# Kernel tuning notes

Measured on AMD Instinct MI355X. Metric: run time of the kernel, lower is better.

Reference implementation:

```python
import jax, jax.numpy as jnp
import numpy as np

N, E, D, K, H = 100000, 1600000, 32, 3, 1


def setup_inputs() -> dict:
    key = jax.random.key(0)
    ks = jax.random.split(key, 7)
    return {
        "src": jax.random.randint(ks[0], (E,), 0, N),
        "dst": jax.random.randint(ks[1], (E,), 0, N),
        "embedding": jax.random.normal(ks[2], (N, D), jnp.float32),
        "lambda_max": jnp.full((1,), 2.0, jnp.float32),
        # ChebConv: single Linear(k*d -> d) over concatenated Chebyshev terms (shared by both calls)
        "cheb_W": jax.random.normal(ks[3], (K * D, D), jnp.float32) / np.sqrt(K * D),
        "cheb_b": jnp.zeros((D,), jnp.float32),
        # GATv2: fc_src / fc_dst Linear(d -> H*d) + attention vector (H, d)
        "gat_W_src": jax.random.normal(ks[4], (D, H * D), jnp.float32) / np.sqrt(D),
        "gat_b_src": jnp.zeros((H * D,), jnp.float32),
        "gat_W_dst": jax.random.normal(ks[5], (D, H * D), jnp.float32) / np.sqrt(D),
        "gat_b_dst": jnp.zeros((H * D,), jnp.float32),
        "gat_attn": jax.random.normal(ks[6], (H, D), jnp.float32) / np.sqrt(D),
    }


def _cheb(src, dst, feat, lam, W, b, n):
    # DGL ChebConv with lambda_max given; activation = leaky_relu (slope 0.01)
    deg = jnp.clip(jax.ops.segment_sum(jnp.ones(src.shape[0], feat.dtype), dst, num_segments=n), 1.0)
    dinv = deg[:, None] ** -0.5  # D^{-1/2}, (N,1)
    re_norm = 2.0 / lam[0]

    def unnL(f):  # D^{-1/2} A D^{-1/2} f
        return jax.ops.segment_sum((f * dinv)[src], dst, num_segments=n) * dinv

    X0 = feat
    X1 = -re_norm * unnL(X0) + X0 * (re_norm - 1.0)
    Xs = [X0, X1]
    for _ in range(2, K):
        Xi = -2.0 * re_norm * unnL(X1) + X1 * (2.0 * (re_norm - 1.0)) - X0
        Xs.append(Xi)
        X0, X1 = X1, Xi
    return jax.nn.leaky_relu(jnp.concatenate(Xs, axis=1) @ W + b, 0.01)


def _gatv2(src, dst, h, Ws, bs, Wd, bd, attn, n):
    Hh, Dd = attn.shape
    fs = (h @ Ws + bs).reshape(n, Hh, Dd)  # feat_src 'el'
    fd = (h @ Wd + bd).reshape(n, Hh, Dd)  # feat_dst 'er'
    e = jax.nn.leaky_relu(fs[src] + fd[dst], 0.2)        # (E,H,D), GATv2 negative_slope=0.2
    logits = jnp.einsum('ehd,hd->eh', e, attn)           # (E,H)
    m = jax.ops.segment_max(logits, dst, num_segments=n)  # per-dst softmax (edge_softmax)
    ex = jnp.exp(logits - m[dst])
    a = ex / jax.ops.segment_sum(ex, dst, num_segments=n)[dst]
    ft = jax.ops.segment_sum(fs[src] * a[..., None], dst, num_segments=n)  # (N,H,D)
    return jax.nn.leaky_relu(ft, 0.01)  # activation=F.leaky_relu


def reference(src, dst, embedding, lambda_max, cheb_W, cheb_b,
              gat_W_src, gat_b_src, gat_W_dst, gat_b_dst, gat_attn):
    n, d = embedding.shape
    h = _cheb(src, dst, embedding, lambda_max, cheb_W, cheb_b, n)
    h = _cheb(src, dst, h, lambda_max, cheb_W, cheb_b, n)
    out = _gatv2(src, dst, h, gat_W_src, gat_b_src, gat_W_dst, gat_b_dst, gat_attn, n)
    return out.reshape(-1, d)
```

## Files before the change

### kernel.cpp

```cpp
#include <hip/hip_runtime.h>

#define TPB 256
#define TPB2 512
#define NB 512
#define CAPB 4096
#define CHUNK 4096

__global__ void k_zero_u(unsigned int* p, int n){
  int i = blockIdx.x*TPB + threadIdx.x;
  if(i < n) p[i] = 0u;
}

__global__ __launch_bounds__(TPB2) void k_bin1(const int* __restrict__ src,
    const int* __restrict__ dst,
    unsigned int* __restrict__ btail, unsigned int* __restrict__ binned,
    int E, int npb){
  __shared__ unsigned int hist[NB];
  __shared__ unsigned int lofs[NB];
  __shared__ unsigned int base[NB];
  __shared__ unsigned int s[TPB2];
  __shared__ int2 stage[CHUNK];
  int t = threadIdx.x;
  hist[t] = 0u;
  __syncthreads();
  int e0 = blockIdx.x*CHUNK;
  int e1 = e0 + CHUNK; if(e1 > E) e1 = E;
  for(int e = e0 + t; e < e1; e += TPB2)
    atomicAdd(&hist[dst[e]/npb], 1u);
  __syncthreads();
  unsigned int a0 = hist[t];
  s[t] = a0; __syncthreads();
  for(int off = 1; off < TPB2; off <<= 1){
    unsigned int x = (t >= off) ? s[t - off] : 0u;
    __syncthreads();
    s[t] += x;
    __syncthreads();
  }
  unsigned int excl = s[t] - a0;
  lofs[t] = excl;
  base[t] = a0 ? atomicAdd(btail + t, a0) : 0u;
  __syncthreads();
  hist[t] = excl;
  __syncthreads();
  for(int e = e0 + t; e < e1; e += TPB2){
    int d = dst[e];
    int b = d / npb;
    unsigned int p = atomicAdd(&hist[b], 1u);
    stage[p] = make_int2(src[e], d);
  }
  __syncthreads();
  int tot = e1 - e0;
  for(int i = t; i < tot; i += TPB2){
    int2 sd = stage[i];
    int b = sd.y / npb;
    unsigned int go = base[b] + ((unsigned)i - lofs[b]);
    if(go < (unsigned)CAPB)
      binned[(size_t)b*CAPB + go] = ((unsigned)sd.x << 8) | (unsigned)(sd.y - b*npb);
  }
}

__global__ __launch_bounds__(TPB) void k_scanb(const unsigned int* __restrict__ btail,
    unsigned int* __restrict__ bbase, unsigned int* __restrict__ ptr, int N, int E){
  __shared__ unsigned int s[TPB];
  __shared__ unsigned int carry;
  int t = threadIdx.x;
  if(t == 0) carry = 0u;
  __syncthreads();
  for(int base = 0; base < NB; base += TPB){
    unsigned int v = btail[base + t];
    s[t] = v; __syncthreads();
    for(int off = 1; off < TPB; off <<= 1){
      unsigned int x = (t >= off) ? s[t - off] : 0u;
      __syncthreads();
      s[t] += x;
      __syncthreads();
    }
    bbase[base + t] = s[t] - v + carry;
    __syncthreads();
    if(t == 0) carry += s[TPB-1];
    __syncthreads();
  }
  if(t == 0) ptr[N] = (unsigned int)E;
}

__global__ __launch_bounds__(TPB) void k_bin2x(const unsigned int* __restrict__ binned,
    const unsigned int* __restrict__ btail, const unsigned int* __restrict__ bbase,
    unsigned int* __restrict__ ptr, float* __restrict__ dinv,
    int* __restrict__ csr, int npb, int N){
  __shared__ unsigned int ebuf[CAPB];
  __shared__ int obuf[CAPB];
  __shared__ unsigned int cnt_s[256];
  __shared__ unsigned int s[TPB];
  __shared__ unsigned int curs[256];
  int b = blockIdx.x;
  int n0 = b*npb; if(n0 >= N) return;
  int t = threadIdx.x;
  unsigned int cnt = btail[b]; if(cnt > (unsigned)CAPB) cnt = CAPB;
  unsigned int segbase = bbase[b];
  cnt_s[t] = 0u;
  __syncthreads();
  for(unsigned int i = t; i < cnt; i += TPB){
    unsigned int e = binned[(size_t)b*CAPB + i];
    ebuf[i] = e;
    atomicAdd(&cnt_s[e & 255u], 1u);
  }
  __syncthreads();
  unsigned int v = cnt_s[t];
  s[t] = v; __syncthreads();
  for(int off = 1; off < TPB; off <<= 1){
    unsigned int x = (t >= off) ? s[t - off] : 0u;
    __syncthreads();
    s[t] += x;
    __syncthreads();
  }
  unsigned int lo = s[t] - v;
  int n = n0 + t;
  if(t < npb && n < N){
    ptr[n]  = segbase + lo;
    dinv[n] = 1.0f / sqrtf(fmaxf((float)v, 1.0f));
  }
  curs[t] = lo;
  __syncthreads();
  for(unsigned int i = t; i < cnt; i += TPB){
    unsigned int e = ebuf[i];
    unsigned int p = atomicAdd(&curs[e & 255u], 1u);
    obuf[p] = (int)(e >> 8);
  }
  __syncthreads();
  for(unsigned int i = t; i < cnt; i += TPB)
    csr[segbase + i] = obuf[i];
}

__device__ __forceinline__ float4 agg_gather4(const unsigned int* __restrict__ ptr,
    const int* __restrict__ csr,
    const float* __restrict__ X, const float* __restrict__ dinv, int t, int lane){
  int g  = lane >> 3;
  int f4 = (lane & 7) << 2;
  unsigned int p0 = ptr[t], p1 = ptr[t+1];
  float4 S0 = make_float4(0.f,0.f,0.f,0.f);
  float4 S1 = make_float4(0.f,0.f,0.f,0.f);
  for(unsigned int base = p0; base < p1; base += 32){
    int idx = 0; float dva = 0.f;
    unsigned int pos = base + (unsigned)lane;
    if(pos < p1){ idx = csr[pos]; dva = dinv[idx]; }
    unsigned int cnt = p1 - base; if(cnt > 32u) cnt = 32u;
    unsigned int rounds = (cnt + 3u) >> 2;
    for(unsigned int r = 0; r < rounds; r += 2){
      int el0 = (int)(r << 2) + g;
      int s0  = __shfl(idx, el0, 32);
      float d0 = __shfl(dva, el0, 32);
      const float4 x0 = *(const float4*)(X + (size_t)s0*32 + f4);
      if(r + 1 < rounds){
        int el1 = el0 + 4;
        int s1  = __shfl(idx, el1, 32);
        float d1 = __shfl(dva, el1, 32);
        const float4 x1 = *(const float4*)(X + (size_t)s1*32 + f4);
        S1.x += x1.x*d1; S1.y += x1.y*d1; S1.z += x1.z*d1; S1.w += x1.w*d1;
      }
      S0.x += x0.x*d0; S0.y += x0.y*d0; S0.z += x0.z*d0; S0.w += x0.w*d0;
    }
  }
  float4 S;
  S.x = S0.x + S1.x; S.y = S0.y + S1.y; S.z = S0.z + S1.z; S.w = S0.w + S1.w;
  S.x += __shfl_xor(S.x, 8, 32);  S.y += __shfl_xor(S.y, 8, 32);
  S.z += __shfl_xor(S.z, 8, 32);  S.w += __shfl_xor(S.w, 8, 32);
  S.x += __shfl_xor(S.x, 16, 32); S.y += __shfl_xor(S.y, 16, 32);
  S.z += __shfl_xor(S.z, 16, 32); S.w += __shfl_xor(S.w, 16, 32);
  return S;
}

__global__ __launch_bounds__(TPB) void k_cheb1(const unsigned int* __restrict__ ptr,
    const int* __restrict__ csr,
    const float* __restrict__ X0, const float* __restrict__ dinv,
    const float* __restrict__ lam, float* __restrict__ X1, int N){
  int t = blockIdx.x*8 + (threadIdx.x >> 5);
  if(t >= N) return;
  int lane = threadIdx.x & 31;
  float4 S = agg_gather4(ptr, csr, X0, dinv, t, lane);
  if((lane >> 3) != 0) return;
  int f4 = (lane & 7) << 2;
  float re = 2.0f / lam[0];
  float dt = dinv[t];
  size_t o = (size_t)t*32 + f4;
  const float4 x0 = *(const float4*)(X0 + o);
  float4 r;
  r.x = -re*(S.x*dt) + (re-1.0f)*x0.x;
  r.y = -re*(S.y*dt) + (re-1.0f)*x0.y;
  r.z = -re*(S.z*dt) + (re-1.0f)*x0.z;
  r.w = -re*(S.w*dt) + (re-1.0f)*x0.w;
  *(float4*)(X1 + o) = r;
}

__global__ __launch_bounds__(TPB) void k_cheb2(const unsigned int* __restrict__ ptr,
    const int* __restrict__ csr,
    const float* __restrict__ X0, const float* __restrict__ X1,
    const float* __restrict__ dinv, const float* __restrict__ lam,
    float* __restrict__ X2, int N){
  int t = blockIdx.x*8 + (threadIdx.x >> 5);
  if(t >= N) return;
  int lane = threadIdx.x & 31;
  float4 S = agg_gather4(ptr, csr, X1, dinv, t, lane);
  if((lane >> 3) != 0) return;
  int f4 = (lane & 7) << 2;
  float re = 2.0f / lam[0];
  float dt = dinv[t];
  size_t o = (size_t)t*32 + f4;
  const float4 x0 = *(const float4*)(X0 + o);
  const float4 x1 = *(const float4*)(X1 + o);
  float c1 = -2.0f*re, c2 = 2.0f*(re-1.0f);
  float4 r;
  r.x = c1*(S.x*dt) + c2*x1.x - x0.x;
  r.y = c1*(S.y*dt) + c2*x1.y - x0.y;
  r.z = c1*(S.z*dt) + c2*x1.z - x0.z;
  r.w = c1*(S.w*dt) + c2*x1.w - x0.w;
  *(float4*)(X2 + o) = r;
}

__global__ __launch_bounds__(TPB) void k_lin(const float* __restrict__ X0,
    const float* __restrict__ X1,
    const float* __restrict__ X2, const float* __restrict__ W,
    const float* __restrict__ b, float* __restrict__ out, int N){
  int n = blockIdx.x*TPB + threadIdx.x;
  if(n >= N) return;
  float acc[32];
  #pragma unroll
  for(int c = 0; c < 32; c++) acc[c] = b[c];
  const float* xs0 = X0 + (size_t)n*32;
  const float* xs1 = X1 + (size_t)n*32;
  const float* xs2 = X2 + (size_t)n*32;
  #pragma unroll
  for(int s3 = 0; s3 < 3; s3++){
    const float4* xp = (const float4*)(s3 == 0 ? xs0 : (s3 == 1 ? xs1 : xs2));
    #pragma unroll
    for(int q = 0; q < 8; q++){
      float4 xv = xp[q];
      const float* Wr = W + (size_t)(s3*32 + q*4)*32;
      #pragma unroll
      for(int c = 0; c < 32; c++)
        acc[c] += xv.x*Wr[c] + xv.y*Wr[32+c] + xv.z*Wr[64+c] + xv.w*Wr[96+c];
    }
  }
  float4* op = (float4*)(out + (size_t)n*32);
  #pragma unroll
  for(int q = 0; q < 8; q++){
    float4 v;
    float a;
    a = acc[4*q+0]; v.x = a > 0.f ? a : 0.01f*a;
    a = acc[4*q+1]; v.y = a > 0.f ? a : 0.01f*a;
    a = acc[4*q+2]; v.z = a > 0.f ? a : 0.01f*a;
    a = acc[4*q+3]; v.w = a > 0.f ? a : 0.01f*a;
    op[q] = v;
  }
}

__global__ __launch_bounds__(TPB) void k_fc(const float* __restrict__ h,
    const float* __restrict__ Wsr, const float* __restrict__ bsr,
    const float* __restrict__ Wds, const float* __restrict__ bds,
    float* __restrict__ fs, float* __restrict__ fd, int N){
  int n = blockIdx.x*TPB + threadIdx.x;
  if(n >= N) return;
  float as[32], ad[32];
  #pragma unroll
  for(int c = 0; c < 32; c++){ as[c] = bsr[c]; ad[c] = bds[c]; }
  const float4* xp = (const float4*)(h + (size_t)n*32);
  #pragma unroll
  for(int q = 0; q < 8; q++){
    float4 xv = xp[q];
    const float* Wr = Wsr + (size_t)(q*4)*32;
    const float* Vr = Wds + (size_t)(q*4)*32;
    #pragma unroll
    for(int c = 0; c < 32; c++){
      as[c] += xv.x*Wr[c] + xv.y*Wr[32+c] + xv.z*Wr[64+c] + xv.w*Wr[96+c];
      ad[c] += xv.x*Vr[c] + xv.y*Vr[32+c] + xv.z*Vr[64+c] + xv.w*Vr[96+c];
    }
  }
  float4* sp = (float4*)(fs + (size_t)n*32);
  float4* dp = (float4*)(fd + (size_t)n*32);
  #pragma unroll
  for(int q = 0; q < 8; q++){
    float4 v1, v2;
    v1.x = as[4*q+0]; v1.y = as[4*q+1]; v1.z = as[4*q+2]; v1.w = as[4*q+3];
    v2.x = ad[4*q+0]; v2.y = ad[4*q+1]; v2.z = ad[4*q+2]; v2.w = ad[4*q+3];
    sp[q] = v1;
    dp[q] = v2;
  }
}

__global__ __launch_bounds__(TPB) void k_gat(const unsigned int* __restrict__ ptr,
    const int* __restrict__ csr,
    const float* __restrict__ fs, const float* __restrict__ fd,
    const float* __restrict__ attn, float* __restrict__ out, int N){
  int t = blockIdx.x*8 + (threadIdx.x >> 5);
  if(t >= N) return;
  int lane = threadIdx.x & 31;
  int g  = lane >> 3;
  int f4 = (lane & 7) << 2;
  unsigned int p0 = ptr[t], p1 = ptr[t+1];
  const float4 fd4 = *(const float4*)(fd + (size_t)t*32 + f4);
  const float4 at4 = *(const float4*)(attn + f4);
  float m = -3.402823466e38f, den = 0.f;
  float4 acc = make_float4(0.f,0.f,0.f,0.f);
  for(unsigned int base = p0; base < p1; base += 32){
    int idx = 0;
    unsigned int pos = base + (unsigned)lane;
    if(pos < p1) idx = csr[pos];
    unsigned int cnt = p1 - base; if(cnt > 32u) cnt = 32u;
    unsigned int rounds = (cnt + 3u) >> 2;
    for(unsigned int r = 0; r < rounds; r++){
      int el = (int)(r << 2) + g;
      int s  = __shfl(idx, el, 32);
      const float4 f = *(const float4*)(fs + (size_t)s*32 + f4);
      float vx = f.x + fd4.x; vx = vx > 0.f ? vx : 0.2f*vx;
      float vy = f.y + fd4.y; vy = vy > 0.f ? vy : 0.2f*vy;
      float vz = f.z + fd4.z; vz = vz > 0.f ? vz : 0.2f*vz;
      float vw = f.w + fd4.w; vw = vw > 0.f ? vw : 0.2f*vw;
      float pl = vx*at4.x + vy*at4.y + vz*at4.z + vw*at4.w;
      pl += __shfl_xor(pl, 4, 32);
      pl += __shfl_xor(pl, 2, 32);
      pl += __shfl_xor(pl, 1, 32);
      if(el < (int)cnt){
        float mn = fmaxf(m, pl);
        float sc = __expf(m - mn);
        float e  = __expf(pl - mn);
        den = den*sc + e;
        acc.x = acc.x*sc + f.x*e;
        acc.y = acc.y*sc + f.y*e;
        acc.z = acc.z*sc + f.z*e;
        acc.w = acc.w*sc + f.w*e;
        m = mn;
      }
    }
  }
  #pragma unroll
  for(int off = 8; off <= 16; off <<= 1){
    float mo = __shfl_xor(m, off, 32);
    float do_ = __shfl_xor(den, off, 32);
    float ax = __shfl_xor(acc.x, off, 32);
    float ay = __shfl_xor(acc.y, off, 32);
    float az = __shfl_xor(acc.z, off, 32);
    float aw = __shfl_xor(acc.w, off, 32);
    float mn = fmaxf(m, mo);
    float a = __expf(m - mn), b = __expf(mo - mn);
    den = den*a + do_*b;
    acc.x = acc.x*a + ax*b;
    acc.y = acc.y*a + ay*b;
    acc.z = acc.z*a + az*b;
    acc.w = acc.w*a + aw*b;
    m = mn;
  }
  if(g != 0) return;
  float4 o = make_float4(0.f,0.f,0.f,0.f);
  if(den > 0.f){
    float inv = 1.0f / den;
    o.x = acc.x*inv; o.x = o.x > 0.f ? o.x : 0.01f*o.x;
    o.y = acc.y*inv; o.y = o.y > 0.f ? o.y : 0.01f*o.y;
    o.z = acc.z*inv; o.z = o.z > 0.f ? o.z : 0.01f*o.z;
    o.w = acc.w*inv; o.w = o.w > 0.f ? o.w : 0.01f*o.w;
  }
  *(float4*)(out + (size_t)t*32 + f4) = o;
}

extern "C" void kernel_launch(void* const* d_in, const int* in_sizes, int n_in,
                              void* d_out, int out_size, void* d_ws, size_t ws_size,
                              hipStream_t stream){
  const int*   src = (const int*)d_in[0];
  const int*   dst = (const int*)d_in[1];
  const float* emb = (const float*)d_in[2];
  const float* lam = (const float*)d_in[3];
  const float* cW  = (const float*)d_in[4];
  const float* cB  = (const float*)d_in[5];
  const float* gWs = (const float*)d_in[6];
  const float* gbs = (const float*)d_in[7];
  const float* gWd = (const float*)d_in[8];
  const float* gbd = (const float*)d_in[9];
  const float* gat = (const float*)d_in[10];
  const int E  = in_sizes[0];
  const int N  = in_sizes[2] / 32;
  const int NF = N * 32;
  const int npb = (N + NB - 1) / NB;

  int gN  = (N + TPB-1)/TPB;
  int gR  = (N + 7)/8;
  int gB1 = (E + CHUNK-1)/CHUNK;

  char* p = (char*)d_ws;
  auto alloc = [&](size_t bytes)->char*{ char* r = p; p += (bytes + 255) & ~(size_t)255; return r; };
  unsigned int* ptrA = (unsigned int*)alloc((size_t)(N+1)*4);
  unsigned int* btail= (unsigned int*)alloc((size_t)NB*4);
  unsigned int* bbase= (unsigned int*)alloc((size_t)NB*4);
  float* dinv = (float*)alloc((size_t)N*4);
  int*   csr  = (int*)alloc((size_t)E*4);
  float* X1   = (float*)alloc((size_t)NF*4);
  float* X2   = (float*)alloc((size_t)NF*4);
  float* h1   = (float*)alloc((size_t)NF*4);
  float* h2   = (float*)alloc((size_t)NF*4);
  unsigned int* binned = (unsigned int*)X1;

  k_zero_u<<<(NB+TPB-1)/TPB, TPB, 0, stream>>>(btail, NB);
  k_bin1<<<gB1, TPB2, 0, stream>>>(src, dst, btail, binned, E, npb);
  k_scanb<<<1, TPB, 0, stream>>>(btail, bbase, ptrA, N, E);
  k_bin2x<<<NB, TPB, 0, stream>>>(binned, btail, bbase, ptrA, dinv, csr, npb, N);

  k_cheb1<<<gR, TPB, 0, stream>>>(ptrA, csr, emb, dinv, lam, X1, N);
  k_cheb2<<<gR, TPB, 0, stream>>>(ptrA, csr, emb, X1, dinv, lam, X2, N);
  k_lin<<<gN, TPB, 0, stream>>>(emb, X1, X2, cW, cB, h1, N);

  k_cheb1<<<gR, TPB, 0, stream>>>(ptrA, csr, h1, dinv, lam, X1, N);
  k_cheb2<<<gR, TPB, 0, stream>>>(ptrA, csr, h1, X1, dinv, lam, X2, N);
  k_lin<<<gN, TPB, 0, stream>>>(h1, X1, X2, cW, cB, h2, N);

  k_fc<<<gN, TPB, 0, stream>>>(h2, gWs, gbs, gWd, gbd, X1 , X2 , N);
  k_gat<<<gR, TPB, 0, stream>>>(ptrA, csr, X1, X2, gat, (float*)d_out, N);
}
```

Before: 366.2 us.

## Restructure dense linear kernels to wave-per-node with register-resident weights

```diff
diff --git a/kernel.cpp b/kernel.cpp
--- a/kernel.cpp
+++ b/kernel.cpp
@@ -5,6 +5,7 @@
 #define NB 512
 #define CAPB 4096
 #define CHUNK 4096
+#define GW 1024
 
 __global__ void k_zero_u(unsigned int* p, int n){
   int i = blockIdx.x*TPB + threadIdx.x;
@@ -220,36 +221,43 @@
     const float* __restrict__ X1,
     const float* __restrict__ X2, const float* __restrict__ W,
     const float* __restrict__ b, float* __restrict__ out, int N){
-  int n = blockIdx.x*TPB + threadIdx.x;
-  if(n >= N) return;
-  float acc[32];
+  int lane = threadIdx.x & 63;
+  int wid  = (blockIdx.x*TPB + threadIdx.x) >> 6;
+  int nw   = (GW*TPB) >> 6;
+  int c  = lane & 31;
+  int kh = lane >> 5;
+  float w[48];
   #pragma unroll
-  for(int c = 0; c < 32; c++) acc[c] = b[c];
-  const float* xs0 = X0 + (size_t)n*32;
-  const float* xs1 = X1 + (size_t)n*32;
-  const float* xs2 = X2 + (size_t)n*32;
-  #pragma unroll
-  for(int s3 = 0; s3 < 3; s3++){
-    const float4* xp = (const float4*)(s3 == 0 ? xs0 : (s3 == 1 ? xs1 : xs2));
+  for(int k = 0; k < 48; k++)
+    w[k] = W[(size_t)(kh*48 + k)*32 + c];
+  float bias = b[c];
+  for(int n = wid; n < N; n += nw){
+    const float4* p0 = (const float4*)(X0 + (size_t)n*32);
+    const float4* p1 = (const float4*)(X1 + (size_t)n*32);
+    const float4* p2 = (const float4*)(X2 + (size_t)n*32);
+    float4 xv[12];
+    if(kh == 0){
+      #pragma unroll
+      for(int i = 0; i < 8; i++) xv[i] = p0[i];
+      #pragma unroll
+      for(int i = 0; i < 4; i++) xv[8+i] = p1[i];
+    } else {
+      #pragma unroll
+      for(int i = 0; i < 4; i++) xv[i] = p1[4+i];
+      #pragma unroll
+      for(int i = 0; i < 8; i++) xv[4+i] = p2[i];
+    }
+    float acc = 0.f;
     #pragma unroll
-    for(int q = 0; q < 8; q++){
-      float4 xv = xp[q];
-      const float* Wr = W + (size_t)(s3*32 + q*4)*32;
-      #pragma unroll
-      for(int c = 0; c < 32; c++)
-        acc[c] += xv.x*Wr[c] + xv.y*Wr[32+c] + xv.z*Wr[64+c] + xv.w*Wr[96+c];
-    }
-  }
-  float4* op = (float4*)(out + (size_t)n*32);
-  #pragma unroll
-  for(int q = 0; q < 8; q++){
-    float4 v;
-    float a;
-    a = acc[4*q+0]; v.x = a > 0.f ? a : 0.01f*a;
-    a = acc[4*q+1]; v.y = a > 0.f ? a : 0.01f*a;
-    a = acc[4*q+2]; v.z = a > 0.f ? a : 0.01f*a;
-    a = acc[4*q+3]; v.w = a > 0.f ? a : 0.01f*a;
-    op[q] = v;
+    for(int i = 0; i < 12; i++){
+      acc += w[4*i+0]*xv[i].x + w[4*i+1]*xv[i].y
+           + w[4*i+2]*xv[i].z + w[4*i+3]*xv[i].w;
+    }
+    acc += __shfl_xor(acc, 32, 64);
+    if(kh == 0){
+      float a = acc + bias;
+      out[(size_t)n*32 + c] = a > 0.f ? a : 0.01f*a;
+    }
   }
 }
 
@@ -257,32 +265,37 @@
     const float* __restrict__ Wsr, const float* __restrict__ bsr,
     const float* __restrict__ Wds, const float* __restrict__ bds,
     float* __restrict__ fs, float* __restrict__ fd, int N){
-  int n = blockIdx.x*TPB + threadIdx.x;
-  if(n >= N) return;
-  float as[32], ad[32];
+  int lane = threadIdx.x & 63;
+  int wid  = (blockIdx.x*TPB + threadIdx.x) >> 6;
+  int nw   = (GW*TPB) >> 6;
+  int c  = lane & 31;
+  int kh = lane >> 5;
+  float ws[16], wd[16];
   #pragma unroll
-  for(int c = 0; c < 32; c++){ as[c] = bsr[c]; ad[c] = bds[c]; }
-  const float4* xp = (const float4*)(h + (size_t)n*32);
-  #pragma unroll
-  for(int q = 0; q < 8; q++){
-    float4 xv = xp[q];
-    const float* Wr = Wsr + (size_t)(q*4)*32;
-    const float* Vr = Wds + (size_t)(q*4)*32;
+  for(int k = 0; k < 16; k++){
+    ws[k] = Wsr[(size_t)(kh*16 + k)*32 + c];
+    wd[k] = Wds[(size_t)(kh*16 + k)*32 + c];
+  }
+  float bs = bsr[c], bd = bds[c];
+  for(int n = wid; n < N; n += nw){
+    const float4* ph = (const float4*)(h + (size_t)n*32) + kh*4;
+    float4 hv[4];
     #pragma unroll
-    for(int c = 0; c < 32; c++){
-      as[c] += xv.x*Wr[c] + xv.y*Wr[32+c] + xv.z*Wr[64+c] + xv.w*Wr[96+c];
-      ad[c] += xv.x*Vr[c] + xv.y*Vr[32+c] + xv.z*Vr[64+c] + xv.w*Vr[96+c];
-    }
-  }
-  float4* sp = (float4*)(fs + (size_t)n*32);
-  float4* dp = (float4*)(fd + (size_t)n*32);
-  #pragma unroll
-  for(int q = 0; q < 8; q++){
-    float4 v1, v2;
-    v1.x = as[4*q+0]; v1.y = as[4*q+1]; v1.z = as[4*q+2]; v1.w = as[4*q+3];
-    v2.x = ad[4*q+0]; v2.y = ad[4*q+1]; v2.z = ad[4*q+2]; v2.w = ad[4*q+3];
-    sp[q] = v1;
-    dp[q] = v2;
+    for(int i = 0; i < 4; i++) hv[i] = ph[i];
+    float as = 0.f, ad = 0.f;
+    #pragma unroll
+    for(int i = 0; i < 4; i++){
+      as += ws[4*i+0]*hv[i].x + ws[4*i+1]*hv[i].y
+          + ws[4*i+2]*hv[i].z + ws[4*i+3]*hv[i].w;
+      ad += wd[4*i+0]*hv[i].x + wd[4*i+1]*hv[i].y
+          + wd[4*i+2]*hv[i].z + wd[4*i+3]*hv[i].w;
+    }
+    as += __shfl_xor(as, 32, 64);
+    ad += __shfl_xor(ad, 32, 64);
+    if(kh == 0){
+      fs[(size_t)n*32 + c] = as + bs;
+      fd[(size_t)n*32 + c] = ad + bd;
+    }
   }
 }
 
@@ -379,7 +392,6 @@
   const int NF = N * 32;
   const int npb = (N + NB - 1) / NB;
 
-  int gN  = (N + TPB-1)/TPB;
   int gR  = (N + 7)/8;
   int gB1 = (E + CHUNK-1)/CHUNK;
 
@@ -403,12 +415,12 @@
 
   k_cheb1<<<gR, TPB, 0, stream>>>(ptrA, csr, emb, dinv, lam, X1, N);
   k_cheb2<<<gR, TPB, 0, stream>>>(ptrA, csr, emb, X1, dinv, lam, X2, N);
-  k_lin<<<gN, TPB, 0, stream>>>(emb, X1, X2, cW, cB, h1, N);
+  k_lin<<<GW, TPB, 0, stream>>>(emb, X1, X2, cW, cB, h1, N);
 
   k_cheb1<<<gR, TPB, 0, stream>>>(ptrA, csr, h1, dinv, lam, X1, N);
   k_cheb2<<<gR, TPB, 0, stream>>>(ptrA, csr, h1, X1, dinv, lam, X2, N);
-  k_lin<<<gN, TPB, 0, stream>>>(h1, X1, X2, cW, cB, h2, N);
-
-  k_fc<<<gN, TPB, 0, stream>>>(h2, gWs, gbs, gWd, gbd, X1 , X2 , N);
+  k_lin<<<GW, TPB, 0, stream>>>(h1, X1, X2, cW, cB, h2, N);
+
+  k_fc<<<GW, TPB, 0, stream>>>(h2, gWs, gbs, gWd, gbd, X1 , X2 , N);
   k_gat<<<gR, TPB, 0, stream>>>(ptrA, csr, X1, X2, gat, (float*)d_out, N);
 }
```

Result: slower. 405.0 us (+10.6%).
